# Optimization experiments

Hardware: AMD Instinct MI355X
Metric: run time of the kernel (lower is better)

The kernel has to match this reference:

```python
import jax, jax.numpy as jnp
import numpy as np
import math

EMBED = 64
HEADS = 2
HEAD_DIM = EMBED // HEADS
B = 262144
EPS = 1e-5


def _linear_params(key, fan_in, fan_out):
    kw, kb = jax.random.split(key)
    bound = 1.0 / math.sqrt(fan_in)
    W = jax.random.uniform(kw, (fan_out, fan_in), jnp.float32, -bound, bound)
    b = jax.random.uniform(kb, (fan_out,), jnp.float32, -bound, bound)
    return W, b


def setup_inputs() -> dict:
    key = jax.random.key(0)
    ks = jax.random.split(key, 12)
    v1 = jax.random.normal(ks[0], (B, EMBED), jnp.float32)
    v2 = jax.random.normal(ks[1], (B, EMBED), jnp.float32)
    Wq1, bq1 = _linear_params(ks[2], EMBED, EMBED)
    Wk2, bk2 = _linear_params(ks[3], EMBED, EMBED)
    Wv2, bv2 = _linear_params(ks[4], EMBED, EMBED)
    Wo1, bo1 = _linear_params(ks[5], EMBED, EMBED)
    Wq2, bq2 = _linear_params(ks[6], EMBED, EMBED)
    Wk1, bk1 = _linear_params(ks[7], EMBED, EMBED)
    Wv1, bv1 = _linear_params(ks[8], EMBED, EMBED)
    Wo2, bo2 = _linear_params(ks[9], EMBED, EMBED)
    g1 = jnp.ones((EMBED,), jnp.float32); be1 = jnp.zeros((EMBED,), jnp.float32)
    g2 = jnp.ones((EMBED,), jnp.float32); be2 = jnp.zeros((EMBED,), jnp.float32)
    return dict(v1_embed=v1, v2_embed=v2,
                Wq1=Wq1, bq1=bq1, Wk2=Wk2, bk2=bk2, Wv2=Wv2, bv2=bv2, Wo1=Wo1, bo1=bo1,
                Wq2=Wq2, bq2=bq2, Wk1=Wk1, bk1=bk1, Wv1=Wv1, bv1=bv1, Wo2=Wo2, bo2=bo2,
                g1=g1, be1=be1, g2=g2, be2=be2)


def _lin(x, W, b):
    return x @ W.T + b


def _mha_single_token(q, k, v):
    # q,k,v: (B, EMBED); one query token, one key token per batch element.
    Bq = q.shape[0]
    Q = q.reshape(Bq, HEADS, HEAD_DIM)
    K = k.reshape(Bq, HEADS, HEAD_DIM)
    V = v.reshape(Bq, HEADS, HEAD_DIM)
    scores = jnp.sum(Q * K, axis=-1, keepdims=True) / jnp.sqrt(jnp.float32(HEAD_DIM))  # (B,H,1)
    w = jax.nn.softmax(scores[..., None], axis=-1)[..., 0]  # softmax over length-1 key axis -> 1.0
    attended = w * V  # (B,H,HEAD_DIM)
    return attended.reshape(Bq, EMBED)


def _layernorm(x, g, b):
    mu = jnp.mean(x, axis=-1, keepdims=True)
    var = jnp.mean(jnp.square(x - mu), axis=-1, keepdims=True)
    return (x - mu) * jax.lax.rsqrt(var + EPS) * g + b


def reference(v1_embed, v2_embed, Wq1, bq1, Wk2, bk2, Wv2, bv2, Wo1, bo1,
              Wq2, bq2, Wk1, bk1, Wv1, bv1, Wo2, bo2, g1, be1, g2, be2):
    # v1 attends to v2
    q1p = _lin(v1_embed, Wq1, bq1)
    k2p = _lin(v2_embed, Wk2, bk2)
    v2p = _lin(v2_embed, Wv2, bv2)
    a1 = _lin(_mha_single_token(q1p, k2p, v2p), Wo1, bo1)
    a1 = _layernorm(a1 + v1_embed, g1, be1)
    # v2 attends to v1
    q2p = _lin(v2_embed, Wq2, bq2)
    k1p = _lin(v1_embed, Wk1, bk1)
    v1p = _lin(v1_embed, Wv1, bv1)
    a2 = _lin(_mha_single_token(q2p, k1p, v1p), Wo2, bo2)
    a2 = _layernorm(a2 + v2_embed, g2, be2)
    return a1, a2
```

## Files before the change

kernel.cpp:

```cpp
#include <hip/hip_runtime.h>

typedef unsigned short u16;
typedef short v8s __attribute__((ext_vector_type(8)));
typedef float f4 __attribute__((ext_vector_type(4)));

#define NROWS 262144
#define UNITS 8
#define TSTRIDE 2048

__device__ __forceinline__ u16 f2bf(float f) {
  union { float f; unsigned int i; } x; x.f = f;
  unsigned int r = x.i + 0x7fffu + ((x.i >> 16) & 1u);
  return (u16)(r >> 16);
}

typedef const __attribute__((address_space(1))) float* gp1;
typedef __attribute__((address_space(3))) float* lp3;
__device__ __forceinline__ void g2l16(const float* g, float* l) {
  __builtin_amdgcn_global_load_lds((gp1)g, (lp3)l, 16, 0, 0);
}

#define FENCE_LGKM0() asm volatile("s_waitcnt lgkmcnt(0)" ::: "memory")
#define FENCE_VM(n)   asm volatile("s_waitcnt vmcnt(" #n ")" ::: "memory")

__global__ void fuse_weights(const float* __restrict__ Wo1, const float* __restrict__ Wv2,
                             const float* __restrict__ bv2, const float* __restrict__ bo1,
                             const float* __restrict__ Wo2, const float* __restrict__ Wv1,
                             const float* __restrict__ bv1, const float* __restrict__ bo2,
                             const float* __restrict__ g1,  const float* __restrict__ be1,
                             const float* __restrict__ g2,  const float* __restrict__ be2,
                             u16* __restrict__ M1, u16* __restrict__ M2,
                             float* __restrict__ cgb) {
  int item = blockIdx.x * 256 + threadIdx.x;
  int mat = item >> 10;
  int n   = (item >> 4) & 63;
  int k0  = (item & 15) * 4;
  const float* Wo = mat ? Wo2 : Wo1;
  const float* Wv = mat ? Wv1 : Wv2;
  float a0 = 0.f, a1 = 0.f, a2 = 0.f, a3 = 0.f;
  for (int j = 0; j < 64; ++j) {
    float w = Wo[n * 64 + j];
    f4 wv = *(const f4*)(Wv + j * 64 + k0);
    a0 += w * wv[0];
    a1 += w * wv[1];
    a2 += w * wv[2];
    a3 += w * wv[3];
  }
  u16* M = mat ? M2 : M1;
  M[n * 64 + k0 + 0] = f2bf(a0);
  M[n * 64 + k0 + 1] = f2bf(a1);
  M[n * 64 + k0 + 2] = f2bf(a2);
  M[n * 64 + k0 + 3] = f2bf(a3);
  if ((item & 15) == 0) {
    const float* bv = mat ? bv1 : bv2;
    const float* bo = mat ? bo2 : bo1;
    float s = bo[n];
    for (int j = 0; j < 64; ++j) s += Wo[n * 64 + j] * bv[j];
    cgb[mat * 64 + n] = s;
    const float* g  = mat ? g2 : g1;
    const float* be = mat ? be2 : be1;
    cgb[128 + mat * 128 + n] = g[n];
    cgb[192 + mat * 128 + n] = be[n];
  }
}

__global__ __launch_bounds__(256, 2) void xattn(
    const float* __restrict__ v1, const float* __restrict__ v2,
    const u16* __restrict__ M1, const u16* __restrict__ M2,
    const float* __restrict__ cgb,
    float* __restrict__ out1, float* __restrict__ out2) {
  const int lane = threadIdx.x & 63;
  const int wave = threadIdx.x >> 6;
  const int quad = lane >> 4;
  const int l15  = lane & 15;
  const int path = wave & 1;

  __shared__ float sbuf[4][2][2][1024];
  __shared__ float scgb[384];
  if (threadIdx.x < 96)
    ((f4*)scgb)[threadIdx.x] = ((const f4*)cgb)[threadIdx.x];

  const u16*   M    = path ? M2  : M1;
  const float* xsrc = path ? v1  : v2;
  const float* rsrc = path ? v2  : v1;
  float*       outp = path ? out2 : out1;
  const int coff = path * 64;
  const int goff = 128 + path * 128;
  const int boff = 192 + path * 128;

  __syncthreads();

  v8s a[4][2];
#pragma unroll
  for (int mt = 0; mt < 4; ++mt)
#pragma unroll
    for (int ks = 0; ks < 2; ++ks)
      a[mt][ks] = *(const v8s*)(M + (mt * 16 + l15) * 64 + ks * 32 + quad * 8);

  const int unit0 = blockIdx.x * 2 + (wave >> 1);

  const int soff = (lane >> 4) * 64 + (lane & 15) * 4;

  auto stage = [&](int buf, int tile) {
    const size_t rbase = (size_t)tile * 16;
    const float* xg = xsrc + rbase * 64 + soff;
    const float* rg = rsrc + rbase * 64 + soff;
    float* xl = &sbuf[wave][buf][0][0];
    float* rl = &sbuf[wave][buf][1][0];
#pragma unroll
    for (int j = 0; j < 4; ++j) {
      g2l16(xg + j * 256, xl + j * 256);
      g2l16(rg + j * 256, rl + j * 256);
    }
  };

  stage(0, unit0);
  stage(1, unit0 + TSTRIDE);

#pragma unroll
  for (int it = 0; it < UNITS; ++it) {
    const int buf = it & 1;

    if (it > 0 && it + 1 < UNITS) {
      FENCE_LGKM0();
      stage(buf ^ 1, unit0 + (it + 1) * TSTRIDE);
    }

    if (it == 0)              { FENCE_VM(8); }
    else if (it == UNITS - 1) { FENCE_VM(4); }
    else                      { FENCE_VM(12); }

    const float* xw = &sbuf[wave][buf][0][0];
    const float* rw = &sbuf[wave][buf][1][0];
    f4 x0 = *(const f4*)(xw + l15 * 64 + quad * 8);
    f4 x1 = *(const f4*)(xw + l15 * 64 + quad * 8 + 4);
    f4 x2 = *(const f4*)(xw + l15 * 64 + quad * 8 + 32);
    f4 x3 = *(const f4*)(xw + l15 * 64 + quad * 8 + 36);
    f4 rv[4];
#pragma unroll
    for (int mt = 0; mt < 4; ++mt)
      rv[mt] = *(const f4*)(rw + l15 * 64 + mt * 16 + quad * 4);

    v8s b0, b1;
#pragma unroll
    for (int j = 0; j < 4; ++j) {
      b0[j]     = (short)f2bf(x0[j]);
      b0[j + 4] = (short)f2bf(x1[j]);
      b1[j]     = (short)f2bf(x2[j]);
      b1[j + 4] = (short)f2bf(x3[j]);
    }

    f4 acc[4];
#pragma unroll
    for (int mt = 0; mt < 4; ++mt) {
      f4 c = {0.f, 0.f, 0.f, 0.f};
      c = __builtin_amdgcn_mfma_f32_16x16x32_bf16(a[mt][0], b0, c, 0, 0, 0);
      c = __builtin_amdgcn_mfma_f32_16x16x32_bf16(a[mt][1], b1, c, 0, 0, 0);
      acc[mt] = c;
    }

    float sum = 0.f, sq = 0.f;
#pragma unroll
    for (int mt = 0; mt < 4; ++mt) {
      const int fo = mt * 16 + quad * 4;
      f4 cf = *(const f4*)(scgb + coff + fo);
#pragma unroll
      for (int j = 0; j < 4; ++j) {
        float t = acc[mt][j] + cf[j] + rv[mt][j];
        acc[mt][j] = t;
        sum += t;
        sq  += t * t;
      }
    }
    sum += __shfl_xor(sum, 16, 64);
    sq  += __shfl_xor(sq,  16, 64);
    sum += __shfl_xor(sum, 32, 64);
    sq  += __shfl_xor(sq,  32, 64);
    float mean = sum * 0.015625f;
    float var  = sq * 0.015625f - mean * mean;
    float rstd = rsqrtf(var + 1e-5f);

    const size_t r0 = (size_t)(unit0 + it * TSTRIDE) * 16;
    float* orow = outp + (r0 + l15) * 64 + quad * 4;
#pragma unroll
    for (int mt = 0; mt < 4; ++mt) {
      const int fo = mt * 16 + quad * 4;
      f4 g  = *(const f4*)(scgb + goff + fo);
      f4 be = *(const f4*)(scgb + boff + fo);
      f4 o;
#pragma unroll
      for (int j = 0; j < 4; ++j)
        o[j] = (acc[mt][j] - mean) * rstd * g[j] + be[j];
      *(f4*)(orow + mt * 16) = o;
    }
  }
}

extern "C" void kernel_launch(void* const* d_in, const int* in_sizes, int n_in,
                              void* d_out, int out_size, void* d_ws, size_t ws_size,
                              hipStream_t stream) {
  const float* v1  = (const float*)d_in[0];
  const float* v2  = (const float*)d_in[1];
  const float* Wv2 = (const float*)d_in[6];
  const float* bv2 = (const float*)d_in[7];
  const float* Wo1 = (const float*)d_in[8];
  const float* bo1 = (const float*)d_in[9];
  const float* Wv1 = (const float*)d_in[14];
  const float* bv1 = (const float*)d_in[15];
  const float* Wo2 = (const float*)d_in[16];
  const float* bo2 = (const float*)d_in[17];
  const float* g1  = (const float*)d_in[18];
  const float* be1 = (const float*)d_in[19];
  const float* g2  = (const float*)d_in[20];
  const float* be2 = (const float*)d_in[21];

  u16* M1 = (u16*)d_ws;
  u16* M2 = M1 + 4096;
  float* cgb = (float*)((char*)d_ws + 16384);

  float* out1 = (float*)d_out;
  float* out2 = out1 + (size_t)NROWS * 64;

  fuse_weights<<<8, 256, 0, stream>>>(Wo1, Wv2, bv2, bo1, Wo2, Wv1, bv1, bo2,
                                      g1, be1, g2, be2, M1, M2, cgb);
  xattn<<<1024, 256, 0, stream>>>(v1, v2, M1, M2, cgb, out1, out2);
}
```

Baseline: 281.9 us.

## Process both attention paths per wave to load each input tile once

Each wave now computes both output paths for its 16-row tile instead of splitting them across two waves. Previously two waves each staged the same v1 and v2 tile, so every input was read from global memory twice. The grid is halved so coverage stays the same, and the LDS row stride is padded (260 floats per four-row group) to reduce bank conflicts on the fragment reads. In exchange, each wave holds weight fragments for both matrices, which raises register pressure, and does twice the compute per wave with fewer waves in flight.

```diff
diff --git a/kernel.cpp b/kernel.cpp
--- a/kernel.cpp
+++ b/kernel.cpp
@@ -73,73 +73,50 @@
   const int wave = threadIdx.x >> 6;
   const int quad = lane >> 4;
   const int l15  = lane & 15;
-  const int path = wave & 1;
-
-  __shared__ float sbuf[4][2][2][1024];
+
+  __shared__ float sbuf[4][2][2][1040];
   __shared__ float scgb[384];
   if (threadIdx.x < 96)
     ((f4*)scgb)[threadIdx.x] = ((const f4*)cgb)[threadIdx.x];
-
-  const u16*   M    = path ? M2  : M1;
-  const float* xsrc = path ? v1  : v2;
-  const float* rsrc = path ? v2  : v1;
-  float*       outp = path ? out2 : out1;
-  const int coff = path * 64;
-  const int goff = 128 + path * 128;
-  const int boff = 192 + path * 128;
-
   __syncthreads();
 
-  v8s a[4][2];
+  v8s a1[4][2], a2[4][2];
 #pragma unroll
   for (int mt = 0; mt < 4; ++mt)
 #pragma unroll
-    for (int ks = 0; ks < 2; ++ks)
-      a[mt][ks] = *(const v8s*)(M + (mt * 16 + l15) * 64 + ks * 32 + quad * 8);
-
-  const int unit0 = blockIdx.x * 2 + (wave >> 1);
-
-  const int soff = (lane >> 4) * 64 + (lane & 15) * 4;
+    for (int ks = 0; ks < 2; ++ks) {
+      a1[mt][ks] = *(const v8s*)(M1 + (mt * 16 + l15) * 64 + ks * 32 + quad * 8);
+      a2[mt][ks] = *(const v8s*)(M2 + (mt * 16 + l15) * 64 + ks * 32 + quad * 8);
+    }
+
+  const int t0 = blockIdx.x * 4 + wave;
+  const int ro = (l15 >> 2) * 260 + (l15 & 3) * 64;
 
   auto stage = [&](int buf, int tile) {
-    const size_t rbase = (size_t)tile * 16;
-    const float* xg = xsrc + rbase * 64 + soff;
-    const float* rg = rsrc + rbase * 64 + soff;
-    float* xl = &sbuf[wave][buf][0][0];
-    float* rl = &sbuf[wave][buf][1][0];
+    const float* gp1v = v1 + (size_t)tile * 1024 + lane * 4;
+    const float* gp2v = v2 + (size_t)tile * 1024 + lane * 4;
+    float* l1 = &sbuf[wave][buf][0][0];
+    float* l2 = &sbuf[wave][buf][1][0];
 #pragma unroll
     for (int j = 0; j < 4; ++j) {
-      g2l16(xg + j * 256, xl + j * 256);
-      g2l16(rg + j * 256, rl + j * 256);
+      g2l16(gp1v + j * 256, l1 + j * 260);
+      g2l16(gp2v + j * 256, l2 + j * 260);
     }
   };
 
-  stage(0, unit0);
-  stage(1, unit0 + TSTRIDE);
-
-#pragma unroll
-  for (int it = 0; it < UNITS; ++it) {
-    const int buf = it & 1;
-
-    if (it > 0 && it + 1 < UNITS) {
-      FENCE_LGKM0();
-      stage(buf ^ 1, unit0 + (it + 1) * TSTRIDE);
-    }
-
-    if (it == 0)              { FENCE_VM(8); }
-    else if (it == UNITS - 1) { FENCE_VM(4); }
-    else                      { FENCE_VM(12); }
-
-    const float* xw = &sbuf[wave][buf][0][0];
-    const float* rw = &sbuf[wave][buf][1][0];
-    f4 x0 = *(const f4*)(xw + l15 * 64 + quad * 8);
-    f4 x1 = *(const f4*)(xw + l15 * 64 + quad * 8 + 4);
-    f4 x2 = *(const f4*)(xw + l15 * 64 + quad * 8 + 32);
-    f4 x3 = *(const f4*)(xw + l15 * 64 + quad * 8 + 36);
+  stage(0, t0);
+  stage(1, t0 + TSTRIDE);
+
+  auto dopath = [&](const v8s (&am)[4][2], const float* xw, const float* rw,
+                    int coff, int goff, int boff, float* outp, size_t r0) {
+    f4 x0 = *(const f4*)(xw + ro + quad * 8);
+    f4 x1 = *(const f4*)(xw + ro + quad * 8 + 4);
+    f4 x2 = *(const f4*)(xw + ro + quad * 8 + 32);
+    f4 x3 = *(const f4*)(xw + ro + quad * 8 + 36);
     f4 rv[4];
 #pragma unroll
     for (int mt = 0; mt < 4; ++mt)
-      rv[mt] = *(const f4*)(rw + l15 * 64 + mt * 16 + quad * 4);
+      rv[mt] = *(const f4*)(rw + ro + mt * 16 + quad * 4);
 
     v8s b0, b1;
 #pragma unroll
@@ -154,8 +131,8 @@
 #pragma unroll
     for (int mt = 0; mt < 4; ++mt) {
       f4 c = {0.f, 0.f, 0.f, 0.f};
-      c = __builtin_amdgcn_mfma_f32_16x16x32_bf16(a[mt][0], b0, c, 0, 0, 0);
-      c = __builtin_amdgcn_mfma_f32_16x16x32_bf16(a[mt][1], b1, c, 0, 0, 0);
+      c = __builtin_amdgcn_mfma_f32_16x16x32_bf16(am[mt][0], b0, c, 0, 0, 0);
+      c = __builtin_amdgcn_mfma_f32_16x16x32_bf16(am[mt][1], b1, c, 0, 0, 0);
       acc[mt] = c;
     }
 
@@ -180,7 +157,6 @@
     float var  = sq * 0.015625f - mean * mean;
     float rstd = rsqrtf(var + 1e-5f);
 
-    const size_t r0 = (size_t)(unit0 + it * TSTRIDE) * 16;
     float* orow = outp + (r0 + l15) * 64 + quad * 4;
 #pragma unroll
     for (int mt = 0; mt < 4; ++mt) {
@@ -193,6 +169,26 @@
         o[j] = (acc[mt][j] - mean) * rstd * g[j] + be[j];
       *(f4*)(orow + mt * 16) = o;
     }
+  };
+
+#pragma unroll
+  for (int it = 0; it < UNITS; ++it) {
+    const int buf = it & 1;
+
+    if (it > 0 && it + 1 < UNITS) {
+      FENCE_LGKM0();
+      stage(buf ^ 1, t0 + (it + 1) * TSTRIDE);
+    }
+
+    if (it == 0 || it == UNITS - 1) { FENCE_VM(8); }
+    else                            { FENCE_VM(16); }
+
+    const float* w1 = &sbuf[wave][buf][0][0];
+    const float* w2 = &sbuf[wave][buf][1][0];
+    const size_t r0 = (size_t)(t0 + it * TSTRIDE) * 16;
+
+    dopath(a1, w2, w1, 0, 128, 192, out1, r0);
+    dopath(a2, w1, w2, 64, 256, 320, out2, r0);
   }
 }
 
@@ -223,5 +219,5 @@
 
   fuse_weights<<<8, 256, 0, stream>>>(Wo1, Wv2, bv2, bo1, Wo2, Wv1, bv1, bo2,
                                       g1, be1, g2, be2, M1, M2, cgb);
-  xattn<<<1024, 256, 0, stream>>>(v1, v2, M1, M2, cgb, out1, out2);
-}
+  xattn<<<512, 256, 0, stream>>>(v1, v2, M1, M2, cgb, out1, out2);
+}
```

Result: no change. 277.9 us (-1.4%).

## Single-buffer shared staging with padded LDS rows and higher occupancy

Applied to the files above, without the earlier changes.

Replaces the double-buffered per-wave LDS staging with one buffer per wave. The next tile's loads are issued right after the current tile's data is read into registers. LDS rows are padded (260-float stride) to reduce bank conflicts, and waves in a block now alternate between the two paths over a shared tile. Less LDS per block lets launch bounds ask for 4 blocks per CU for more latency hiding. The trade-off is a shallower per-wave prefetch in exchange for more concurrent waves.

```diff
diff --git a/kernel.cpp b/kernel.cpp
--- a/kernel.cpp
+++ b/kernel.cpp
@@ -64,7 +64,7 @@
   }
 }
 
-__global__ __launch_bounds__(256, 2) void xattn(
+__global__ __launch_bounds__(256, 4) void xattn(
     const float* __restrict__ v1, const float* __restrict__ v2,
     const u16* __restrict__ M1, const u16* __restrict__ M2,
     const float* __restrict__ cgb,
@@ -73,23 +73,25 @@
   const int wave = threadIdx.x >> 6;
   const int quad = lane >> 4;
   const int l15  = lane & 15;
-  const int path = wave & 1;
-
-  __shared__ float sbuf[4][2][2][1024];
+
+  const int w    = blockIdx.x * 4 + wave;
+  const int path = w & 1;
+  const int t0   = w >> 1;
+
+  __shared__ float sbuf[4][2][1040];
   __shared__ float scgb[384];
   if (threadIdx.x < 96)
     ((f4*)scgb)[threadIdx.x] = ((const f4*)cgb)[threadIdx.x];
-
-  const u16*   M    = path ? M2  : M1;
-  const float* xsrc = path ? v1  : v2;
-  const float* rsrc = path ? v2  : v1;
-  float*       outp = path ? out2 : out1;
+  __syncthreads();
+
+  const u16* M  = path ? M2 : M1;
+  float*   outp = path ? out2 : out1;
+  const int xi  = path ^ 1;
+  const int ri  = path;
   const int coff = path * 64;
   const int goff = 128 + path * 128;
   const int boff = 192 + path * 128;
 
-  __syncthreads();
-
   v8s a[4][2];
 #pragma unroll
   for (int mt = 0; mt < 4; ++mt)
@@ -97,49 +99,41 @@
     for (int ks = 0; ks < 2; ++ks)
       a[mt][ks] = *(const v8s*)(M + (mt * 16 + l15) * 64 + ks * 32 + quad * 8);
 
-  const int unit0 = blockIdx.x * 2 + (wave >> 1);
-
-  const int soff = (lane >> 4) * 64 + (lane & 15) * 4;
-
-  auto stage = [&](int buf, int tile) {
-    const size_t rbase = (size_t)tile * 16;
-    const float* xg = xsrc + rbase * 64 + soff;
-    const float* rg = rsrc + rbase * 64 + soff;
-    float* xl = &sbuf[wave][buf][0][0];
-    float* rl = &sbuf[wave][buf][1][0];
+  const int ro = (l15 >> 2) * 260 + (l15 & 3) * 64;
+
+  auto stage = [&](int tile) {
+    const float* g1v = v1 + (size_t)tile * 1024 + lane * 4;
+    const float* g2v = v2 + (size_t)tile * 1024 + lane * 4;
+    float* l1 = &sbuf[wave][0][0];
+    float* l2 = &sbuf[wave][1][0];
 #pragma unroll
     for (int j = 0; j < 4; ++j) {
-      g2l16(xg + j * 256, xl + j * 256);
-      g2l16(rg + j * 256, rl + j * 256);
+      g2l16(g1v + j * 256, l1 + j * 260);
+      g2l16(g2v + j * 256, l2 + j * 260);
     }
   };
 
-  stage(0, unit0);
-  stage(1, unit0 + TSTRIDE);
+  stage(t0);
 
 #pragma unroll
   for (int it = 0; it < UNITS; ++it) {
-    const int buf = it & 1;
-
-    if (it > 0 && it + 1 < UNITS) {
-      FENCE_LGKM0();
-      stage(buf ^ 1, unit0 + (it + 1) * TSTRIDE);
-    }
-
-    if (it == 0)              { FENCE_VM(8); }
-    else if (it == UNITS - 1) { FENCE_VM(4); }
-    else                      { FENCE_VM(12); }
-
-    const float* xw = &sbuf[wave][buf][0][0];
-    const float* rw = &sbuf[wave][buf][1][0];
-    f4 x0 = *(const f4*)(xw + l15 * 64 + quad * 8);
-    f4 x1 = *(const f4*)(xw + l15 * 64 + quad * 8 + 4);
-    f4 x2 = *(const f4*)(xw + l15 * 64 + quad * 8 + 32);
-    f4 x3 = *(const f4*)(xw + l15 * 64 + quad * 8 + 36);
+    if (it == 0) { FENCE_VM(0); }
+    else         { FENCE_VM(4); }
+
+    const float* xw = &sbuf[wave][xi][0];
+    const float* rw = &sbuf[wave][ri][0];
+    f4 x0 = *(const f4*)(xw + ro + quad * 8);
+    f4 x1 = *(const f4*)(xw + ro + quad * 8 + 4);
+    f4 x2 = *(const f4*)(xw + ro + quad * 8 + 32);
+    f4 x3 = *(const f4*)(xw + ro + quad * 8 + 36);
     f4 rv[4];
 #pragma unroll
     for (int mt = 0; mt < 4; ++mt)
-      rv[mt] = *(const f4*)(rw + l15 * 64 + mt * 16 + quad * 4);
+      rv[mt] = *(const f4*)(rw + ro + mt * 16 + quad * 4);
+
+    FENCE_LGKM0();
+    if (it + 1 < UNITS) stage(t0 + (it + 1) * TSTRIDE);
+    __builtin_amdgcn_sched_barrier(0);
 
     v8s b0, b1;
 #pragma unroll
@@ -180,7 +174,7 @@
     float var  = sq * 0.015625f - mean * mean;
     float rstd = rsqrtf(var + 1e-5f);
 
-    const size_t r0 = (size_t)(unit0 + it * TSTRIDE) * 16;
+    const size_t r0 = (size_t)(t0 + it * TSTRIDE) * 16;
     float* orow = outp + (r0 + l15) * 64 + quad * 4;
 #pragma unroll
     for (int mt = 0; mt < 4; ++mt) {
```

After: 282.7 us. No clear change (+0.3%).
